# Kernel tuning notes

Measured on AMD Instinct MI355X. Metric: run time of the kernel, lower is better.

The kernel has to match this reference:

```python
import jax, jax.numpy as jnp
import numpy as np

REF_CHANNEL = 0
DIAG_EPS = 1e-7   # diag_loading coefficient
TIK_EPS = 1e-8    # additive eps in diagonal loading / trace denominator
MASK_EPS = 1e-15  # PSD mask-normalization eps


def _psd(spec, mask):
    # spec: (b, c, f, t) complex; mask: (b, f, t) real
    # PSD module: normalize mask over time, weight outer products, sum over t.
    m = mask / (mask.sum(axis=-1, keepdims=True) + MASK_EPS)
    return jnp.einsum('bcft,beft,bft->bfce', spec, spec.conj(), m.astype(spec.dtype))


def setup_inputs() -> dict:
    key = jax.random.key(0)
    k1, k2, k3, k4 = jax.random.split(key, 4)
    B, C, F, T = 4, 6, 257, 2000
    return {
        'spec_real': jax.random.normal(k1, (B, C, F, T), dtype=jnp.float32),
        'spec_imag': jax.random.normal(k2, (B, C, F, T), dtype=jnp.float32),
        'mask_s': jax.random.uniform(k3, (B, F, T), dtype=jnp.float32),
        'mask_n': jax.random.uniform(k4, (B, F, T), dtype=jnp.float32),
    }


def reference(spec_real, spec_imag, mask_s, mask_n):
    spec = spec_real + 1j * spec_imag                     # (b, c, f, t) complex64
    C = spec.shape[1]

    psd_s = _psd(spec, mask_s)                            # (b, f, c, c)
    psd_n = _psd(spec, mask_n)                            # (b, f, c, c)

    # Diagonal loading (Tikhonov regularization) of the noise PSD.
    tr_n = jnp.einsum('bfcc->bf', psd_n).real
    epsilon = jax.lax.stop_gradient(tr_n * DIAG_EPS + TIK_EPS)   # torch uses no_grad here
    psd_n = psd_n + epsilon[..., None, None] * jnp.eye(C, dtype=spec.dtype)

    # ref_channel solution: w = (psd_n^-1 psd_s) / trace(psd_n^-1 psd_s) @ u
    numerator = jnp.linalg.solve(psd_n, psd_s)            # (b, f, c, c)
    tr = jnp.einsum('bfcc->bf', numerator)
    ws = numerator / (tr[..., None, None] + TIK_EPS)
    w = ws[..., :, REF_CHANNEL]                           # one-hot u selects column -> (b, f, c)

    # enhanced = w^H Y
    enh = jnp.einsum('bfc,bcft->bft', w.conj(), spec)     # (b, f, t) complex
    return jnp.stack([enh.real, enh.imag], axis=-1)       # (b, f, t, 2) float32
```

## Files before the change

### kernel.cpp

```cpp
#include <hip/hip_runtime.h>

#define NB 4
#define NC 6
#define NF 257
#define NT 2000
#define NPAIR 15
#define NACC 74
#define BLK 256

__global__ __launch_bounds__(BLK, 2) void mvdr_kernel(
    const float* __restrict__ sr, const float* __restrict__ si,
    const float* __restrict__ ms, const float* __restrict__ mn,
    float* __restrict__ out)
{
    constexpr int PC[NPAIR] = {0,0,0,0,0,1,1,1,1,2,2,2,3,3,4};
    constexpr int PE[NPAIR] = {1,2,3,4,5,2,3,4,5,3,4,5,4,5,5};

    const int bf = blockIdx.x;
    const int b  = bf / NF;
    const int f  = bf - b * NF;
    const int CS = NF * NT;
    const int sb = b * NC * CS + f * NT;
    const int mb = (b * NF + f) * NT;

    float acc[NACC];
    #pragma unroll
    for (int i = 0; i < NACC; i++) acc[i] = 0.f;

    for (int t = threadIdx.x; t < NT; t += BLK) {
        const float vms = ms[mb + t];
        const float vmn = mn[mb + t];
        acc[72] += vms;
        acc[73] += vmn;
        float re[NC], im[NC];
        #pragma unroll
        for (int c = 0; c < NC; c++) {
            re[c] = sr[sb + c * CS + t];
            im[c] = si[sb + c * CS + t];
        }
        #pragma unroll
        for (int c = 0; c < NC; c++) {
            const float d = re[c] * re[c] + im[c] * im[c];
            acc[c]     += d * vms;
            acc[6 + c] += d * vmn;
        }
        #pragma unroll
        for (int p = 0; p < NPAIR; p++) {
            const int c = PC[p], e = PE[p];
            const float cr = re[c] * re[e] + im[c] * im[e];
            const float ci = im[c] * re[e] - re[c] * im[e];
            acc[12 + 4 * p + 0] += cr * vms;
            acc[12 + 4 * p + 1] += ci * vms;
            acc[12 + 4 * p + 2] += cr * vmn;
            acc[12 + 4 * p + 3] += ci * vmn;
        }
    }

    #pragma unroll
    for (int i = 0; i < NACC; i++) {
        float v = acc[i];
        v += __shfl_down(v, 32);
        v += __shfl_down(v, 16);
        v += __shfl_down(v, 8);
        v += __shfl_down(v, 4);
        v += __shfl_down(v, 2);
        v += __shfl_down(v, 1);
        acc[i] = v;
    }

    __shared__ float red[4][NACC];
    __shared__ float s_wr[NC], s_wi[NC];
    const int wid  = threadIdx.x >> 6;
    const int lane = threadIdx.x & 63;
    if (lane == 0) {
        #pragma unroll
        for (int i = 0; i < NACC; i++) red[wid][i] = acc[i];
    }
    __syncthreads();

    if (threadIdx.x == 0) {
        #define FIN(i) (red[0][i] + red[1][i] + red[2][i] + red[3][i])
        const float invS = 1.f / (FIN(72) + 1e-15f);
        const float invN = 1.f / (FIN(73) + 1e-15f);

        float Ar[NC][NC], Ai[NC][NC], Br[NC][NC], Bi[NC][NC];
        #pragma unroll
        for (int c = 0; c < NC; c++) {
            Br[c][c] = FIN(c) * invS;     Bi[c][c] = 0.f;
            Ar[c][c] = FIN(6 + c) * invN; Ai[c][c] = 0.f;
        }
        #pragma unroll
        for (int p = 0; p < NPAIR; p++) {
            const int c = PC[p], e = PE[p];
            const float sre = FIN(12 + 4 * p + 0) * invS;
            const float sim = FIN(12 + 4 * p + 1) * invS;
            const float nre = FIN(12 + 4 * p + 2) * invN;
            const float nim = FIN(12 + 4 * p + 3) * invN;
            Br[c][e] = sre;  Bi[c][e] = sim;
            Br[e][c] = sre;  Bi[e][c] = -sim;
            Ar[c][e] = nre;  Ai[c][e] = nim;
            Ar[e][c] = nre;  Ai[e][c] = -nim;
        }
        #undef FIN

        float trn = 0.f;
        #pragma unroll
        for (int c = 0; c < NC; c++) trn += Ar[c][c];
        const float eps = trn * 1e-7f + 1e-8f;
        #pragma unroll
        for (int c = 0; c < NC; c++) Ar[c][c] += eps;

        #pragma unroll
        for (int k = 0; k < NC; k++) {
            const float dr = Ar[k][k], di = Ai[k][k];
            const float idn = 1.f / (dr * dr + di * di);
            const float pr = dr * idn, pi = -di * idn;
            #pragma unroll
            for (int i2 = k + 1; i2 < NC; i2++) {
                const float fr = Ar[i2][k] * pr - Ai[i2][k] * pi;
                const float fi = Ar[i2][k] * pi + Ai[i2][k] * pr;
                #pragma unroll
                for (int j = k + 1; j < NC; j++) {
                    Ar[i2][j] -= fr * Ar[k][j] - fi * Ai[k][j];
                    Ai[i2][j] -= fr * Ai[k][j] + fi * Ar[k][j];
                }
                #pragma unroll
                for (int j = 0; j < NC; j++) {
                    Br[i2][j] -= fr * Br[k][j] - fi * Bi[k][j];
                    Bi[i2][j] -= fr * Bi[k][j] + fi * Br[k][j];
                }
            }
        }
        #pragma unroll
        for (int k = NC - 1; k >= 0; k--) {
            const float dr = Ar[k][k], di = Ai[k][k];
            const float idn = 1.f / (dr * dr + di * di);
            const float pr = dr * idn, pi = -di * idn;
            #pragma unroll
            for (int j = 0; j < NC; j++) {
                float xr = Br[k][j], xi = Bi[k][j];
                #pragma unroll
                for (int m = k + 1; m < NC; m++) {
                    xr -= Ar[k][m] * Br[m][j] - Ai[k][m] * Bi[m][j];
                    xi -= Ar[k][m] * Bi[m][j] + Ai[k][m] * Br[m][j];
                }
                Br[k][j] = xr * pr - xi * pi;
                Bi[k][j] = xr * pi + xi * pr;
            }
        }

        float trr = 1e-8f, tri = 0.f;
        #pragma unroll
        for (int c = 0; c < NC; c++) { trr += Br[c][c]; tri += Bi[c][c]; }
        const float idn = 1.f / (trr * trr + tri * tri);
        #pragma unroll
        for (int c = 0; c < NC; c++) {
            const float xr = Br[c][0], xi = Bi[c][0];
            const float wre = (xr * trr + xi * tri) * idn;
            const float wim = (xi * trr - xr * tri) * idn;
            s_wr[c] = wre;
            s_wi[c] = -wim;
        }
    }
    __syncthreads();

    float wr[NC], wi[NC];
    #pragma unroll
    for (int c = 0; c < NC; c++) { wr[c] = s_wr[c]; wi[c] = s_wi[c]; }

    float2* o2 = (float2*)out;
    for (int t = threadIdx.x; t < NT; t += BLK) {
        float er = 0.f, ei = 0.f;
        #pragma unroll
        for (int c = 0; c < NC; c++) {
            const float a  = sr[sb + c * CS + t];
            const float bb = si[sb + c * CS + t];
            er += wr[c] * a - wi[c] * bb;
            ei += wr[c] * bb + wi[c] * a;
        }
        o2[mb + t] = make_float2(er, ei);
    }
}

extern "C" void kernel_launch(void* const* d_in, const int* in_sizes, int n_in,
                              void* d_out, int out_size, void* d_ws, size_t ws_size,
                              hipStream_t stream) {
    const float* sr = (const float*)d_in[0];
    const float* si = (const float*)d_in[1];
    const float* ms = (const float*)d_in[2];
    const float* mn = (const float*)d_in[3];
    float* out = (float*)d_out;
    mvdr_kernel<<<NB * NF, BLK, 0, stream>>>(sr, si, ms, mn, out);
}
```

Before: 176.6 us.

## Split MVDR into PSD, batched solve, and apply kernels with time-chunked blocks

Replaces the single fused per-frequency kernel with three kernels. The first accumulates partial PSDs over two time chunks per (b,f) using float2 loads. The second runs the 6x6 complex solve with one thread per (b,f) instead of a serial thread 0 in each block. The third applies the beamformer with float4 stores. This doubles the block count and removes the single-thread solve stall from the streaming kernels. In exchange it adds extra launches, a workspace round trip, and a second full read of the spectrum that is no longer held in cache across phases.

```diff
diff --git a/kernel.cpp b/kernel.cpp
--- a/kernel.cpp
+++ b/kernel.cpp
@@ -4,57 +4,80 @@
 #define NC 6
 #define NF 257
 #define NT 2000
+#define NG (NB * NF)
 #define NPAIR 15
 #define NACC 74
+#define NCHUNK 2
+#define TCH (NT / NCHUNK)
 #define BLK 256
-
-__global__ __launch_bounds__(BLK, 2) void mvdr_kernel(
+#define CS  (NF * NT)
+#define CS2 (CS / 2)
+
+__device__ __forceinline__ void acc_pos(
+    const float2* __restrict__ s2r, const float2* __restrict__ s2i,
+    const float2* __restrict__ m2s, const float2* __restrict__ m2n,
+    int p, float (&acc)[NACC])
+{
+    constexpr int PC[NPAIR] = {0,0,0,0,0,1,1,1,1,2,2,2,3,3,4};
+    constexpr int PE[NPAIR] = {1,2,3,4,5,2,3,4,5,3,4,5,4,5,5};
+
+    const float2 vms = m2s[p];
+    const float2 vmn = m2n[p];
+    acc[72] += vms.x + vms.y;
+    acc[73] += vmn.x + vmn.y;
+
+    float2 re[NC], im[NC];
+    #pragma unroll
+    for (int c = 0; c < NC; c++) {
+        re[c] = s2r[c * CS2 + p];
+        im[c] = s2i[c * CS2 + p];
+    }
+    #pragma unroll
+    for (int c = 0; c < NC; c++) {
+        const float d0 = re[c].x * re[c].x + im[c].x * im[c].x;
+        const float d1 = re[c].y * re[c].y + im[c].y * im[c].y;
+        acc[c]     += d0 * vms.x + d1 * vms.y;
+        acc[6 + c] += d0 * vmn.x + d1 * vmn.y;
+    }
+    #pragma unroll
+    for (int q = 0; q < NPAIR; q++) {
+        const int c = PC[q], e = PE[q];
+        const float cr0 = re[c].x * re[e].x + im[c].x * im[e].x;
+        const float ci0 = im[c].x * re[e].x - re[c].x * im[e].x;
+        const float cr1 = re[c].y * re[e].y + im[c].y * im[e].y;
+        const float ci1 = im[c].y * re[e].y - re[c].y * im[e].y;
+        acc[12 + 4 * q + 0] += cr0 * vms.x + cr1 * vms.y;
+        acc[12 + 4 * q + 1] += ci0 * vms.x + ci1 * vms.y;
+        acc[12 + 4 * q + 2] += cr0 * vmn.x + cr1 * vmn.y;
+        acc[12 + 4 * q + 3] += ci0 * vmn.x + ci1 * vmn.y;
+    }
+}
+
+__global__ __launch_bounds__(BLK) void psd_kernel(
     const float* __restrict__ sr, const float* __restrict__ si,
     const float* __restrict__ ms, const float* __restrict__ mn,
-    float* __restrict__ out)
-{
-    constexpr int PC[NPAIR] = {0,0,0,0,0,1,1,1,1,2,2,2,3,3,4};
-    constexpr int PE[NPAIR] = {1,2,3,4,5,2,3,4,5,3,4,5,4,5,5};
-
-    const int bf = blockIdx.x;
-    const int b  = bf / NF;
-    const int f  = bf - b * NF;
-    const int CS = NF * NT;
-    const int sb = b * NC * CS + f * NT;
-    const int mb = (b * NF + f) * NT;
+    float* __restrict__ wsp)
+{
+    const int bx = blockIdx.x;
+    const int g  = bx >> 1;
+    const int b  = g / NF;
+    const int f  = g - b * NF;
+    const int tb = (bx & 1) * TCH;
+    const int sbase = b * NC * CS + f * NT + tb;
+    const int mbase = g * NT + tb;
+
+    const float2* s2r = (const float2*)(sr + sbase);
+    const float2* s2i = (const float2*)(si + sbase);
+    const float2* m2s = (const float2*)(ms + mbase);
+    const float2* m2n = (const float2*)(mn + mbase);
 
     float acc[NACC];
     #pragma unroll
     for (int i = 0; i < NACC; i++) acc[i] = 0.f;
 
-    for (int t = threadIdx.x; t < NT; t += BLK) {
-        const float vms = ms[mb + t];
-        const float vmn = mn[mb + t];
-        acc[72] += vms;
-        acc[73] += vmn;
-        float re[NC], im[NC];
-        #pragma unroll
-        for (int c = 0; c < NC; c++) {
-            re[c] = sr[sb + c * CS + t];
-            im[c] = si[sb + c * CS + t];
-        }
-        #pragma unroll
-        for (int c = 0; c < NC; c++) {
-            const float d = re[c] * re[c] + im[c] * im[c];
-            acc[c]     += d * vms;
-            acc[6 + c] += d * vmn;
-        }
-        #pragma unroll
-        for (int p = 0; p < NPAIR; p++) {
-            const int c = PC[p], e = PE[p];
-            const float cr = re[c] * re[e] + im[c] * im[e];
-            const float ci = im[c] * re[e] - re[c] * im[e];
-            acc[12 + 4 * p + 0] += cr * vms;
-            acc[12 + 4 * p + 1] += ci * vms;
-            acc[12 + 4 * p + 2] += cr * vmn;
-            acc[12 + 4 * p + 3] += ci * vmn;
-        }
-    }
+    acc_pos(s2r, s2i, m2s, m2n, threadIdx.x, acc);
+    if (threadIdx.x < (TCH / 2 - BLK))
+        acc_pos(s2r, s2i, m2s, m2n, threadIdx.x + BLK, acc);
 
     #pragma unroll
     for (int i = 0; i < NACC; i++) {
@@ -62,123 +85,172 @@
         v += __shfl_down(v, 32);
         v += __shfl_down(v, 16);
         v += __shfl_down(v, 8);
-        v += __shfl_down(v, 4);
-        v += __shfl_down(v, 2);
-        v += __shfl_down(v, 1);
         acc[i] = v;
     }
 
-    __shared__ float red[4][NACC];
-    __shared__ float s_wr[NC], s_wi[NC];
+    __shared__ float red[32][NACC];
     const int wid  = threadIdx.x >> 6;
     const int lane = threadIdx.x & 63;
-    if (lane == 0) {
-        #pragma unroll
-        for (int i = 0; i < NACC; i++) red[wid][i] = acc[i];
+    if (lane < 8) {
+        #pragma unroll
+        for (int i = 0; i < NACC; i++) red[wid * 8 + lane][i] = acc[i];
     }
     __syncthreads();
 
-    if (threadIdx.x == 0) {
-        #define FIN(i) (red[0][i] + red[1][i] + red[2][i] + red[3][i])
-        const float invS = 1.f / (FIN(72) + 1e-15f);
-        const float invN = 1.f / (FIN(73) + 1e-15f);
-
-        float Ar[NC][NC], Ai[NC][NC], Br[NC][NC], Bi[NC][NC];
-        #pragma unroll
-        for (int c = 0; c < NC; c++) {
-            Br[c][c] = FIN(c) * invS;     Bi[c][c] = 0.f;
-            Ar[c][c] = FIN(6 + c) * invN; Ai[c][c] = 0.f;
-        }
-        #pragma unroll
-        for (int p = 0; p < NPAIR; p++) {
-            const int c = PC[p], e = PE[p];
-            const float sre = FIN(12 + 4 * p + 0) * invS;
-            const float sim = FIN(12 + 4 * p + 1) * invS;
-            const float nre = FIN(12 + 4 * p + 2) * invN;
-            const float nim = FIN(12 + 4 * p + 3) * invN;
-            Br[c][e] = sre;  Bi[c][e] = sim;
-            Br[e][c] = sre;  Bi[e][c] = -sim;
-            Ar[c][e] = nre;  Ai[c][e] = nim;
-            Ar[e][c] = nre;  Ai[e][c] = -nim;
-        }
-        #undef FIN
-
-        float trn = 0.f;
-        #pragma unroll
-        for (int c = 0; c < NC; c++) trn += Ar[c][c];
-        const float eps = trn * 1e-7f + 1e-8f;
-        #pragma unroll
-        for (int c = 0; c < NC; c++) Ar[c][c] += eps;
-
-        #pragma unroll
-        for (int k = 0; k < NC; k++) {
-            const float dr = Ar[k][k], di = Ai[k][k];
-            const float idn = 1.f / (dr * dr + di * di);
-            const float pr = dr * idn, pi = -di * idn;
+    if (threadIdx.x < NACC) {
+        float s = 0.f;
+        #pragma unroll
+        for (int r = 0; r < 32; r++) s += red[r][threadIdx.x];
+        wsp[bx * NACC + threadIdx.x] = s;
+    }
+}
+
+__global__ void solve_kernel(const float* __restrict__ wsp, float* __restrict__ wsw)
+{
+    const int gid = blockIdx.x * 64 + threadIdx.x;
+    if (gid >= NG) return;
+
+    constexpr int PC[NPAIR] = {0,0,0,0,0,1,1,1,1,2,2,2,3,3,4};
+    constexpr int PE[NPAIR] = {1,2,3,4,5,2,3,4,5,3,4,5,4,5,5};
+
+    const float* p0 = wsp + (2 * gid) * NACC;
+    const float* p1 = p0 + NACC;
+    float fin[NACC];
+    #pragma unroll
+    for (int i = 0; i < NACC; i++) fin[i] = p0[i] + p1[i];
+
+    const float invS = 1.f / (fin[72] + 1e-15f);
+    const float invN = 1.f / (fin[73] + 1e-15f);
+
+    float Ar[NC][NC], Ai[NC][NC], Br[NC][NC], Bi[NC][NC];
+    #pragma unroll
+    for (int c = 0; c < NC; c++) {
+        Br[c][c] = fin[c] * invS;     Bi[c][c] = 0.f;
+        Ar[c][c] = fin[6 + c] * invN; Ai[c][c] = 0.f;
+    }
+    #pragma unroll
+    for (int q = 0; q < NPAIR; q++) {
+        const int c = PC[q], e = PE[q];
+        const float sre = fin[12 + 4 * q + 0] * invS;
+        const float sim = fin[12 + 4 * q + 1] * invS;
+        const float nre = fin[12 + 4 * q + 2] * invN;
+        const float nim = fin[12 + 4 * q + 3] * invN;
+        Br[c][e] = sre;  Bi[c][e] = sim;
+        Br[e][c] = sre;  Bi[e][c] = -sim;
+        Ar[c][e] = nre;  Ai[c][e] = nim;
+        Ar[e][c] = nre;  Ai[e][c] = -nim;
+    }
+
+    float trn = 0.f;
+    #pragma unroll
+    for (int c = 0; c < NC; c++) trn += Ar[c][c];
+    const float eps = trn * 1e-7f + 1e-8f;
+    #pragma unroll
+    for (int c = 0; c < NC; c++) Ar[c][c] += eps;
+
+    #pragma unroll
+    for (int k = 0; k < NC; k++) {
+        const float dr = Ar[k][k], di = Ai[k][k];
+        const float idn = 1.f / (dr * dr + di * di);
+        const float pr = dr * idn, pi = -di * idn;
+        #pragma unroll
+        for (int i2 = k + 1; i2 < NC; i2++) {
+            const float fr = Ar[i2][k] * pr - Ai[i2][k] * pi;
+            const float fi = Ar[i2][k] * pi + Ai[i2][k] * pr;
             #pragma unroll
-            for (int i2 = k + 1; i2 < NC; i2++) {
-                const float fr = Ar[i2][k] * pr - Ai[i2][k] * pi;
-                const float fi = Ar[i2][k] * pi + Ai[i2][k] * pr;
-                #pragma unroll
-                for (int j = k + 1; j < NC; j++) {
-                    Ar[i2][j] -= fr * Ar[k][j] - fi * Ai[k][j];
-                    Ai[i2][j] -= fr * Ai[k][j] + fi * Ar[k][j];
-                }
-                #pragma unroll
-                for (int j = 0; j < NC; j++) {
-                    Br[i2][j] -= fr * Br[k][j] - fi * Bi[k][j];
-                    Bi[i2][j] -= fr * Bi[k][j] + fi * Br[k][j];
-                }
+            for (int j = k + 1; j < NC; j++) {
+                Ar[i2][j] -= fr * Ar[k][j] - fi * Ai[k][j];
+                Ai[i2][j] -= fr * Ai[k][j] + fi * Ar[k][j];
             }
-        }
-        #pragma unroll
-        for (int k = NC - 1; k >= 0; k--) {
-            const float dr = Ar[k][k], di = Ai[k][k];
-            const float idn = 1.f / (dr * dr + di * di);
-            const float pr = dr * idn, pi = -di * idn;
             #pragma unroll
             for (int j = 0; j < NC; j++) {
-                float xr = Br[k][j], xi = Bi[k][j];
-                #pragma unroll
-                for (int m = k + 1; m < NC; m++) {
-                    xr -= Ar[k][m] * Br[m][j] - Ai[k][m] * Bi[m][j];
-                    xi -= Ar[k][m] * Bi[m][j] + Ai[k][m] * Br[m][j];
-                }
-                Br[k][j] = xr * pr - xi * pi;
-                Bi[k][j] = xr * pi + xi * pr;
+                Br[i2][j] -= fr * Br[k][j] - fi * Bi[k][j];
+                Bi[i2][j] -= fr * Bi[k][j] + fi * Br[k][j];
             }
         }
-
-        float trr = 1e-8f, tri = 0.f;
-        #pragma unroll
-        for (int c = 0; c < NC; c++) { trr += Br[c][c]; tri += Bi[c][c]; }
-        const float idn = 1.f / (trr * trr + tri * tri);
+    }
+    #pragma unroll
+    for (int k = NC - 1; k >= 0; k--) {
+        const float dr = Ar[k][k], di = Ai[k][k];
+        const float idn = 1.f / (dr * dr + di * di);
+        const float pr = dr * idn, pi = -di * idn;
+        #pragma unroll
+        for (int j = 0; j < NC; j++) {
+            float xr = Br[k][j], xi = Bi[k][j];
+            #pragma unroll
+            for (int m = k + 1; m < NC; m++) {
+                xr -= Ar[k][m] * Br[m][j] - Ai[k][m] * Bi[m][j];
+                xi -= Ar[k][m] * Bi[m][j] + Ai[k][m] * Br[m][j];
+            }
+            Br[k][j] = xr * pr - xi * pi;
+            Bi[k][j] = xr * pi + xi * pr;
+        }
+    }
+
+    float trr = 1e-8f, tri = 0.f;
+    #pragma unroll
+    for (int c = 0; c < NC; c++) { trr += Br[c][c]; tri += Bi[c][c]; }
+    const float idn = 1.f / (trr * trr + tri * tri);
+    #pragma unroll
+    for (int c = 0; c < NC; c++) {
+        const float xr = Br[c][0], xi = Bi[c][0];
+        const float wre = (xr * trr + xi * tri) * idn;
+        const float wim = (xi * trr - xr * tri) * idn;
+        wsw[gid * 12 + c]     = wre;
+        wsw[gid * 12 + 6 + c] = -wim;
+    }
+}
+
+__global__ __launch_bounds__(BLK) void apply_kernel(
+    const float* __restrict__ sr, const float* __restrict__ si,
+    const float* __restrict__ wsw, float* __restrict__ out)
+{
+    const int bx = blockIdx.x;
+    const int g  = bx >> 1;
+    const int b  = g / NF;
+    const int f  = g - b * NF;
+    const int tb = (bx & 1) * TCH;
+    const int sbase = b * NC * CS + f * NT + tb;
+
+    const float2* s2r = (const float2*)(sr + sbase);
+    const float2* s2i = (const float2*)(si + sbase);
+
+    float wr[NC], wi[NC];
+    #pragma unroll
+    for (int c = 0; c < NC; c++) {
+        wr[c] = wsw[g * 12 + c];
+        wi[c] = wsw[g * 12 + 6 + c];
+    }
+
+    float4* o4 = (float4*)out + (g * NT + tb) / 2;
+
+    {
+        const int p = threadIdx.x;
+        float er0 = 0.f, ei0 = 0.f, er1 = 0.f, ei1 = 0.f;
         #pragma unroll
         for (int c = 0; c < NC; c++) {
-            const float xr = Br[c][0], xi = Bi[c][0];
-            const float wre = (xr * trr + xi * tri) * idn;
-            const float wim = (xi * trr - xr * tri) * idn;
-            s_wr[c] = wre;
-            s_wi[c] = -wim;
-        }
-    }
-    __syncthreads();
-
-    float wr[NC], wi[NC];
-    #pragma unroll
-    for (int c = 0; c < NC; c++) { wr[c] = s_wr[c]; wi[c] = s_wi[c]; }
-
-    float2* o2 = (float2*)out;
-    for (int t = threadIdx.x; t < NT; t += BLK) {
-        float er = 0.f, ei = 0.f;
+            const float2 a  = s2r[c * CS2 + p];
+            const float2 bb = s2i[c * CS2 + p];
+            er0 += wr[c] * a.x - wi[c] * bb.x;
+            ei0 += wr[c] * bb.x + wi[c] * a.x;
+            er1 += wr[c] * a.y - wi[c] * bb.y;
+            ei1 += wr[c] * bb.y + wi[c] * a.y;
+        }
+        o4[p] = make_float4(er0, ei0, er1, ei1);
+    }
+    if (threadIdx.x < (TCH / 2 - BLK)) {
+        const int p = threadIdx.x + BLK;
+        float er0 = 0.f, ei0 = 0.f, er1 = 0.f, ei1 = 0.f;
         #pragma unroll
         for (int c = 0; c < NC; c++) {
-            const float a  = sr[sb + c * CS + t];
-            const float bb = si[sb + c * CS + t];
-            er += wr[c] * a - wi[c] * bb;
-            ei += wr[c] * bb + wi[c] * a;
-        }
-        o2[mb + t] = make_float2(er, ei);
+            const float2 a  = s2r[c * CS2 + p];
+            const float2 bb = s2i[c * CS2 + p];
+            er0 += wr[c] * a.x - wi[c] * bb.x;
+            ei0 += wr[c] * bb.x + wi[c] * a.x;
+            er1 += wr[c] * a.y - wi[c] * bb.y;
+            ei1 += wr[c] * bb.y + wi[c] * a.y;
+        }
+        o4[p] = make_float4(er0, ei0, er1, ei1);
     }
 }
 
@@ -190,5 +262,11 @@
     const float* ms = (const float*)d_in[2];
     const float* mn = (const float*)d_in[3];
     float* out = (float*)d_out;
-    mvdr_kernel<<<NB * NF, BLK, 0, stream>>>(sr, si, ms, mn, out);
-}
+
+    float* wsp = (float*)d_ws;
+    float* wsw = wsp + NG * NCHUNK * NACC;
+
+    psd_kernel<<<NG * NCHUNK, BLK, 0, stream>>>(sr, si, ms, mn, wsp);
+    solve_kernel<<<(NG + 63) / 64, 64, 0, stream>>>(wsp, wsw);
+    apply_kernel<<<NG * NCHUNK, BLK, 0, stream>>>(sr, si, wsw, out);
+}
```

Result: no change. 178.0 us (+0.8%).
